# Kernel optimization log

Hardware: AMD Instinct MI355X
Metric: run time of the kernel (lower is better)

Reference implementation:

```python
import jax, jax.numpy as jnp
import numpy as np

H = 8
D_MODEL = 512
D_K = D_MODEL // H
NEG = -1e9


def setup_inputs() -> dict:
    key = jax.random.key(0)
    ks = jax.random.split(key, 11)
    B, S = 2, 2048
    scale = 1.0 / np.sqrt(D_MODEL)
    inp = {
        'query': jax.random.normal(ks[0], (B, S, D_MODEL), dtype=jnp.float32),
        'key': jax.random.normal(ks[1], (B, S, D_MODEL), dtype=jnp.float32),
        'value': jax.random.normal(ks[2], (B, S, D_MODEL), dtype=jnp.float32),
        'Wq': jax.random.normal(ks[3], (D_MODEL, D_MODEL), dtype=jnp.float32) * scale,
        'bq': jnp.zeros((D_MODEL,), dtype=jnp.float32),
        'Wk': jax.random.normal(ks[4], (D_MODEL, D_MODEL), dtype=jnp.float32) * scale,
        'bk': jnp.zeros((D_MODEL,), dtype=jnp.float32),
        'Wv': jax.random.normal(ks[5], (D_MODEL, D_MODEL), dtype=jnp.float32) * scale,
        'bv': jnp.zeros((D_MODEL,), dtype=jnp.float32),
        'Wo': jax.random.normal(ks[6], (D_MODEL, D_MODEL), dtype=jnp.float32) * scale,
        'bo': jnp.zeros((D_MODEL,), dtype=jnp.float32),
    }
    return inp


def reference(query, key, value, Wq, bq, Wk, bk, Wv, bv, Wo, bo):
    B, S, _ = query.shape
    # QKV projections (nn.Linear: x @ W.T + b), split into heads -> [B, H, S, D_K]
    def proj(x, W, b):
        return (x @ W.T + b).reshape(B, S, H, D_K).transpose(0, 2, 1, 3)

    q = proj(query, Wq, bq)
    k = proj(key, Wk, bk)
    v = proj(value, Wv, bv)

    scores = jnp.einsum('bhqd,bhkd->bhqk', q, k) / jnp.sqrt(jnp.float32(D_K))
    # diagonal mask (mask=True): token cannot attend to itself
    diag = jnp.eye(S, dtype=bool)
    scores = jnp.where(diag, NEG, scores)

    p_attn = jax.nn.softmax(scores, axis=-1)  # [B, H, S, S]
    x = jnp.einsum('bhqk,bhkd->bhqd', p_attn, v)
    x = x.transpose(0, 2, 1, 3).reshape(B, S, H * D_K)
    return x @ Wo.T + bo
```

## Files before the change

kernel.cpp:

```cpp
#include <hip/hip_runtime.h>
#include <hip/hip_bf16.h>
#include <math.h>

#define NUM_H 8
#define DK    64
#define DM    512
#define SEQ   2048
#define NB    2
#define MROWS (NB*SEQ)

typedef unsigned short u16;
typedef unsigned int   u32;
typedef __attribute__((ext_vector_type(8))) __bf16 bf16x8;
typedef __attribute__((ext_vector_type(4))) short  s16x4;
typedef __attribute__((ext_vector_type(4))) float  f32x4;

__device__ __forceinline__ u16 f2bf(float v) {
    union { __bf16 h; u16 u; } x; x.h = (__bf16)v; return x.u;
}
__device__ __forceinline__ u16 f2h(float v) {
    union { _Float16 h; u16 u; } x; x.h = (_Float16)v; return x.u;
}
__device__ __forceinline__ float h2f(u16 u) {
    union { u16 u; _Float16 h; } x; x.u = u; return (float)x.h;
}
__device__ __forceinline__ bf16x8 ld_bf8(const u16* p) {
    union { uint4 u; bf16x8 v; } t;
    t.u = *(const uint4*)p;
    return t.v;
}
__device__ __forceinline__ uint4 pack8bf(const float* f) {
    uint4 o;
    o.x = (u32)f2bf(f[0]) | ((u32)f2bf(f[1]) << 16);
    o.y = (u32)f2bf(f[2]) | ((u32)f2bf(f[3]) << 16);
    o.z = (u32)f2bf(f[4]) | ((u32)f2bf(f[5]) << 16);
    o.w = (u32)f2bf(f[6]) | ((u32)f2bf(f[7]) << 16);
    return o;
}
__device__ __forceinline__ float fexp2(float x) {
#if defined(__has_builtin) && __has_builtin(__builtin_amdgcn_exp2f)
    return __builtin_amdgcn_exp2f(x);
#else
    return exp2f(x);
#endif
}

__device__ __forceinline__ f32x4 mfma16bf(s16x4 a, s16x4 b, f32x4 c) {
#if defined(__has_builtin) && __has_builtin(__builtin_amdgcn_mfma_f32_16x16x16bf16_1k)
    return __builtin_amdgcn_mfma_f32_16x16x16bf16_1k(a, b, c, 0, 0, 0);
#else
    asm("v_mfma_f32_16x16x16_bf16 %0, %1, %2, %0" : "+v"(c) : "v"(a), "v"(b));
    return c;
#endif
}

__global__ __launch_bounds__(256) void convW(
    const float* __restrict__ Wq, const float* __restrict__ Wk,
    const float* __restrict__ Wv, const float* __restrict__ Wo,
    u16* __restrict__ Wscr)
{
    const int z = blockIdx.y;
    const float* src = (z == 0) ? Wq : (z == 1) ? Wk : (z == 2) ? Wv : Wo;
    u16* dst = Wscr + (size_t)z * 262144;
    int i = (blockIdx.x * 256 + threadIdx.x) * 8;
    float4 a = *(const float4*)(src + i);
    float4 b = *(const float4*)(src + i + 4);
    float f[8] = {a.x, a.y, a.z, a.w, b.x, b.y, b.z, b.w};
    *(uint4*)&dst[i] = pack8bf(f);
}

#define MODE_QK 0
#define MODE_VT 1
#define MODE_FIN 2

template<int MODE, bool INBF>
__device__ __forceinline__ void gemm_core(
    const void* __restrict__ Xv, const u16* __restrict__ Wb,
    const float* __restrict__ bias, void* __restrict__ outv,
    u16* As, u16* Bs, int row0, int col0)
{
    const int tid = threadIdx.x;
    const int lane = tid & 63, w = tid >> 6;
    const int ln15 = lane & 15, quad = lane >> 4;
    const int wm = (w >> 1) * 32, wn = (w & 1) * 32;

    f32x4 acc[2][2];
#pragma unroll
    for (int mt = 0; mt < 2; ++mt)
#pragma unroll
        for (int nt = 0; nt < 2; ++nt) acc[mt][nt] = (f32x4){0.f, 0.f, 0.f, 0.f};

    for (int kt = 0; kt < DM; kt += 64) {
        __syncthreads();
#pragma unroll
        for (int g = 0; g < 2; ++g) {
            int idx = g * 2048 + tid * 8;
            int r = idx >> 6, c = idx & 63;
            if (INBF) {
                *(uint4*)&As[r * 72 + c] =
                    *(const uint4*)((const u16*)Xv + (size_t)(row0 + r) * DM + kt + c);
            } else {
                const float* xp = (const float*)Xv + (size_t)(row0 + r) * DM + kt + c;
                float4 a = *(const float4*)xp;
                float4 b2 = *(const float4*)(xp + 4);
                float f[8] = {a.x, a.y, a.z, a.w, b2.x, b2.y, b2.z, b2.w};
                *(uint4*)&As[r * 72 + c] = pack8bf(f);
            }
        }
#pragma unroll
        for (int g = 0; g < 2; ++g) {
            int idx = g * 2048 + tid * 8;
            int r = idx >> 6, c = idx & 63;
            *(uint4*)&Bs[r * 72 + c] =
                *(const uint4*)(Wb + (size_t)(col0 + r) * DM + kt + c);
        }
        __syncthreads();

#pragma unroll
        for (int ks = 0; ks < 2; ++ks) {
            bf16x8 af[2], bfr[2];
#pragma unroll
            for (int mt = 0; mt < 2; ++mt)
                af[mt] = ld_bf8(&As[(wm + mt * 16 + ln15) * 72 + ks * 32 + quad * 8]);
#pragma unroll
            for (int nt = 0; nt < 2; ++nt)
                bfr[nt] = ld_bf8(&Bs[(wn + nt * 16 + ln15) * 72 + ks * 32 + quad * 8]);
#pragma unroll
            for (int mt = 0; mt < 2; ++mt)
#pragma unroll
                for (int nt = 0; nt < 2; ++nt)
                    acc[mt][nt] = __builtin_amdgcn_mfma_f32_16x16x32_bf16(
                        af[mt], bfr[nt], acc[mt][nt], 0, 0, 0);
        }
    }

    float bc[2];
#pragma unroll
    for (int nt = 0; nt < 2; ++nt) bc[nt] = bias[col0 + wn + nt * 16 + ln15];
    const int h = col0 >> 6;

    if (MODE == MODE_FIN) {
        float* outF = (float*)outv;
#pragma unroll
        for (int mt = 0; mt < 2; ++mt)
#pragma unroll
            for (int r = 0; r < 4; ++r) {
                int m = row0 + wm + mt * 16 + quad * 4 + r;
#pragma unroll
                for (int nt = 0; nt < 2; ++nt)
                    outF[(size_t)m * DM + col0 + wn + nt * 16 + ln15] = acc[mt][nt][r] + bc[nt];
            }
    } else if (MODE == MODE_QK) {
        u16* outB = (u16*)outv;
#pragma unroll
        for (int mt = 0; mt < 2; ++mt)
#pragma unroll
            for (int r = 0; r < 4; ++r) {
                int m = row0 + wm + mt * 16 + quad * 4 + r;
                int b = m >> 11, s2 = m & (SEQ - 1);
#pragma unroll
                for (int nt = 0; nt < 2; ++nt) {
                    int dk = wn + nt * 16 + ln15;
                    outB[((size_t)((b * NUM_H + h) * SEQ + s2)) * DK + dk] =
                        f2bf(acc[mt][nt][r] + bc[nt]);
                }
            }
    } else {
        u16* outB = (u16*)outv;
        __syncthreads();
#pragma unroll
        for (int mt = 0; mt < 2; ++mt)
#pragma unroll
            for (int nt = 0; nt < 2; ++nt) {
                int dk = wn + nt * 16 + ln15;
#pragma unroll
                for (int r = 0; r < 4; ++r) {
                    int sl = wm + mt * 16 + quad * 4 + r;
                    As[dk * 72 + sl] = f2bf(acc[mt][nt][r] + bc[nt]);
                }
            }
        __syncthreads();
        int dk = tid >> 2, ch = (tid & 3) * 16;
        int b = row0 >> 11, s0 = row0 & (SEQ - 1);
        size_t base = ((size_t)((b * NUM_H + h) * DK + dk)) * SEQ + s0 + ch;
        *(uint4*)&outB[base]     = *(const uint4*)&As[dk * 72 + ch];
        *(uint4*)&outB[base + 8] = *(const uint4*)&As[dk * 72 + ch + 8];
    }
}

__global__ __launch_bounds__(256) void qkv_mfma(
    const float* __restrict__ xq, const float* __restrict__ xk, const float* __restrict__ xv,
    const u16* __restrict__ Wscr,
    const float* __restrict__ b0, const float* __restrict__ b1, const float* __restrict__ b2,
    u16* __restrict__ oQ, u16* __restrict__ oK, u16* __restrict__ oVt)
{
    __shared__ u16 As[64 * 72];
    __shared__ u16 Bs[64 * 72];
    const int row0 = blockIdx.x * 64, col0 = blockIdx.y * 64;
    const int z = blockIdx.z;
    const u16* W = Wscr + (size_t)z * 262144;
    if (z == 2)
        gemm_core<MODE_VT, false>(xv, W, b2, oVt, As, Bs, row0, col0);
    else if (z == 0)
        gemm_core<MODE_QK, false>(xq, W, b0, oQ, As, Bs, row0, col0);
    else
        gemm_core<MODE_QK, false>(xk, W, b1, oK, As, Bs, row0, col0);
}

__global__ __launch_bounds__(256) void final_mfma(
    const u16* __restrict__ X, const u16* __restrict__ Wbf,
    const float* __restrict__ bias, float* __restrict__ out)
{
    __shared__ u16 As[64 * 72];
    __shared__ u16 Bs[64 * 72];
    gemm_core<MODE_FIN, true>(X, Wbf, bias, out, As, Bs,
                              blockIdx.x * 64, blockIdx.y * 64);
}

#define LSTR 72
#define SCL2  0.18033688f
#define BIA2 -5.7708020f
__global__ __launch_bounds__(256) void attn_mfma(
    const u16* __restrict__ Qg, const u16* __restrict__ Kg,
    const u16* __restrict__ Vtg, u16* __restrict__ Pd, float* __restrict__ Cl)
{
    __shared__ u16 Klds[64 * LSTR];
    __shared__ u16 Vtlds[64 * LSTR];

    const int tid = threadIdx.x;
    const int lane = tid & 63;
    const int w = tid >> 6;
    const int ln15 = lane & 15;
    const int quad = lane >> 4;
    const int bh = blockIdx.y;
    const int b = bh >> 3, h = bh & 7;
    const int qb = blockIdx.x * 64;
    const int z = blockIdx.z;
    const int k0 = z * (SEQ / 2), k1 = k0 + SEQ / 2;

    const u16* Qp = Qg + (size_t)bh * SEQ * DK;
    const u16* Kp = Kg + (size_t)bh * SEQ * DK;
    const u16* Vp = Vtg + (size_t)bh * DK * SEQ;

    const int myq = w * 16 + ln15;
    const int qrow = qb + myq;
    const bf16x8 qa0 = ld_bf8(&Qp[(size_t)qrow * DK + quad * 8]);
    const bf16x8 qa1 = ld_bf8(&Qp[(size_t)qrow * DK + 32 + quad * 8]);

    const bool mrow = (quad == (ln15 >> 2));
    const int  mr   = ln15 & 3;

    const s16x4 onesb = (s16x4){(short)0x3F80, (short)0x3F80,
                                (short)0x3F80, (short)0x3F80};

    f32x4 O[4];
    f32x4 Lacc = (f32x4){0.f, 0.f, 0.f, 0.f};
#pragma unroll
    for (int nt = 0; nt < 4; ++nt) O[nt] = (f32x4){0.f, 0.f, 0.f, 0.f};

    const int sr = tid >> 3;
    const int scl = (tid & 7) * 8;
    const u16* kp0 = &Kp[(size_t)sr * DK + scl];
    const u16* kp1 = &Kp[(size_t)(sr + 32) * DK + scl];
    const u16* vp0 = &Vp[(size_t)sr * SEQ + scl];
    const u16* vp1 = &Vp[(size_t)(sr + 32) * SEQ + scl];

    uint4 kreg0 = *(const uint4*)&kp0[(size_t)k0 * DK];
    uint4 kreg1 = *(const uint4*)&kp1[(size_t)k0 * DK];
    uint4 vreg0 = *(const uint4*)&vp0[k0];
    uint4 vreg1 = *(const uint4*)&vp1[k0];

    for (int kt = k0; kt < k1; kt += 64) {
        *(uint4*)&Klds[sr * LSTR + scl]         = kreg0;
        *(uint4*)&Klds[(sr + 32) * LSTR + scl]  = kreg1;
        *(uint4*)&Vtlds[sr * LSTR + scl]        = vreg0;
        *(uint4*)&Vtlds[(sr + 32) * LSTR + scl] = vreg1;
        __syncthreads();

        if (kt + 64 < k1) {
            kreg0 = *(const uint4*)&kp0[(size_t)(kt + 64) * DK];
            kreg1 = *(const uint4*)&kp1[(size_t)(kt + 64) * DK];
            vreg0 = *(const uint4*)&vp0[kt + 64];
            vreg1 = *(const uint4*)&vp1[kt + 64];
        }

        const bool diagt = (kt == qb);
        s16x4 pa[4];
#pragma unroll
        for (int nt2 = 0; nt2 < 4; ++nt2) {
            bf16x8 kb0 = ld_bf8(&Klds[(nt2 * 16 + ln15) * LSTR + quad * 8]);
            bf16x8 kb1 = ld_bf8(&Klds[(nt2 * 16 + ln15) * LSTR + 32 + quad * 8]);
            f32x4 zacc = (f32x4){0.f, 0.f, 0.f, 0.f};
            zacc = __builtin_amdgcn_mfma_f32_16x16x32_bf16(kb0, qa0, zacc, 0, 0, 0);
            zacc = __builtin_amdgcn_mfma_f32_16x16x32_bf16(kb1, qa1, zacc, 0, 0, 0);
            union { u16 u[4]; s16x4 v; } pk;
#pragma unroll
            for (int r = 0; r < 4; ++r)
                pk.u[r] = f2bf(fexp2(fmaf(zacc[r], SCL2, BIA2)));
            if (diagt && nt2 == w) {
#pragma unroll
                for (int r = 0; r < 4; ++r)
                    if (mrow && r == mr) pk.u[r] = 0;
            }
            pa[nt2] = pk.v;
        }

        const u16* vb_base = &Vtlds[ln15 * LSTR + quad * 4];
        __builtin_amdgcn_s_setprio(1);
#pragma unroll
        for (int nt2 = 0; nt2 < 4; ++nt2)
            Lacc = mfma16bf(pa[nt2], onesb, Lacc);
#pragma unroll
        for (int nt = 0; nt < 4; ++nt) {
#pragma unroll
            for (int nt2 = 0; nt2 < 4; ++nt2) {
                s16x4 vb = *(const s16x4*)&vb_base[nt * 16 * LSTR + nt2 * 16];
                O[nt] = mfma16bf(pa[nt2], vb, O[nt]);
            }
        }
        __builtin_amdgcn_s_setprio(0);
        __syncthreads();
    }

    if (ln15 == 0) {
#pragma unroll
        for (int r = 0; r < 4; ++r)
            Cl[(size_t)z * 32768 + bh * SEQ + qb + w * 16 + quad * 4 + r] = Lacc[r];
    }

#pragma unroll
    for (int r = 0; r < 4; ++r) {
        int s = qb + w * 16 + quad * 4 + r;
        size_t base = (size_t)z * 2097152 + ((size_t)(b * SEQ + s)) * DM + h * DK;
#pragma unroll
        for (int nt = 0; nt < 4; ++nt)
            Pd[base + nt * 16 + ln15] = f2h(O[nt][r] * 0.015625f);
    }
}

__global__ __launch_bounds__(256) void combine(
    const u16* __restrict__ Pd, const float* __restrict__ Cl, u16* __restrict__ C)
{
    int idx = (blockIdx.x * 256 + threadIdx.x) * 8;
    int row = idx >> 9, col = idx & 511;
    int b = row >> 11, s = row & (SEQ - 1), h = col >> 6;
    int bh = b * NUM_H + h;
    float lsum = Cl[bh * SEQ + s] + Cl[32768 + bh * SEQ + s];
    float sc = 64.f / lsum;
    uint4 u0 = *(const uint4*)&Pd[idx];
    uint4 u1 = *(const uint4*)&Pd[2097152 + idx];
    u32 a0[4] = {u0.x, u0.y, u0.z, u0.w};
    u32 a1[4] = {u1.x, u1.y, u1.z, u1.w};
    float f[8];
#pragma unroll
    for (int j = 0; j < 4; ++j) {
        f[2 * j]     = (h2f((u16)(a0[j] & 0xffff)) + h2f((u16)(a1[j] & 0xffff))) * sc;
        f[2 * j + 1] = (h2f((u16)(a0[j] >> 16))    + h2f((u16)(a1[j] >> 16)))    * sc;
    }
    *(uint4*)&C[idx] = pack8bf(f);
}

extern "C" void kernel_launch(void* const* d_in, const int* in_sizes, int n_in,
                              void* d_out, int out_size, void* d_ws, size_t ws_size,
                              hipStream_t stream) {
    const float* q  = (const float*)d_in[0];
    const float* k  = (const float*)d_in[1];
    const float* v  = (const float*)d_in[2];
    const float* Wq = (const float*)d_in[3];
    const float* bq = (const float*)d_in[4];
    const float* Wk = (const float*)d_in[5];
    const float* bk = (const float*)d_in[6];
    const float* Wv = (const float*)d_in[7];
    const float* bv = (const float*)d_in[8];
    const float* Wo = (const float*)d_in[9];
    const float* bo = (const float*)d_in[10];
    float* out = (float*)d_out;

    const size_t TSZ = (size_t)MROWS * DM;
    u16* Qb  = (u16*)d_ws;
    u16* Kb  = Qb + TSZ;
    u16* Vtb = Qb + 2 * TSZ;
    u16* CbU = Qb + 3 * TSZ;
    float* Cl  = (float*)CbU;
    u16*  Wscr = CbU + 131072;

    u16* Pd = (u16*)d_out;

    dim3 blk(256);
    hipLaunchKernelGGL(convW, dim3(128, 4), blk, 0, stream, Wq, Wk, Wv, Wo, Wscr);
    dim3 gq(MROWS / 64, DM / 64, 3);
    hipLaunchKernelGGL(qkv_mfma, gq, blk, 0, stream,
                       q, k, v, Wscr, bq, bk, bv, Qb, Kb, Vtb);
    dim3 ga(SEQ / 64, NB * NUM_H, 2);
    hipLaunchKernelGGL(attn_mfma, ga, blk, 0, stream, Qb, Kb, Vtb, Pd, Cl);
    hipLaunchKernelGGL(combine, dim3(1024), blk, 0, stream, Pd, Cl, Qb);
    dim3 gf(MROWS / 64, DM / 64);
    hipLaunchKernelGGL(final_mfma, gf, blk, 0, stream, Qb, Wscr + 3 * 262144, bo, out);
}
```

Measured before the change: 151.9 us.

## Split attention keys four ways and fuse split combine into output projection

Raises the key-dimension split of the attention kernel from 2 to 4, which doubles the number of attention blocks for better occupancy. It removes the separate combine kernel by having the output-projection GEMM load the four fp16 partial outputs, sum them with half2 adds, and scale each row by the reciprocal of the summed row denominators while staging the A tile. The cost is more partial-output traffic: four fp16 partial tensors are now written and read back. Summing in fp16 before scaling may also lose some precision. Partials move from the output buffer into workspace.

```diff
diff --git a/kernel.cpp b/kernel.cpp
--- a/kernel.cpp
+++ b/kernel.cpp
@@ -1,5 +1,6 @@
 #include <hip/hip_runtime.h>
 #include <hip/hip_bf16.h>
+#include <hip/hip_fp16.h>
 #include <math.h>
 
 #define NUM_H 8
@@ -8,6 +9,7 @@
 #define SEQ   2048
 #define NB    2
 #define MROWS (NB*SEQ)
+#define NZ    4
 
 typedef unsigned short u16;
 typedef unsigned int   u32;
@@ -20,9 +22,6 @@
 }
 __device__ __forceinline__ u16 f2h(float v) {
     union { _Float16 h; u16 u; } x; x.h = (_Float16)v; return x.u;
-}
-__device__ __forceinline__ float h2f(u16 u) {
-    union { u16 u; _Float16 h; } x; x.u = u; return (float)x.h;
 }
 __device__ __forceinline__ bf16x8 ld_bf8(const u16* p) {
     union { uint4 u; bf16x8 v; } t;
@@ -73,10 +72,11 @@
 #define MODE_VT 1
 #define MODE_FIN 2
 
-template<int MODE, bool INBF>
+template<int MODE>
 __device__ __forceinline__ void gemm_core(
     const void* __restrict__ Xv, const u16* __restrict__ Wb,
-    const float* __restrict__ bias, void* __restrict__ outv,
+    const float* __restrict__ bias, const float* __restrict__ ClP,
+    void* __restrict__ outv,
     u16* As, u16* Bs, int row0, int col0)
 {
     const int tid = threadIdx.x;
@@ -84,6 +84,13 @@
     const int ln15 = lane & 15, quad = lane >> 4;
     const int wm = (w >> 1) * 32, wn = (w & 1) * 32;
 
+    int cb0 = 0, cs0 = 0, cb1 = 0, cs1 = 0;
+    if (MODE == MODE_FIN) {
+        int m0 = row0 + (tid >> 3), m1 = m0 + 32;
+        cb0 = (m0 >> 11) * NUM_H; cs0 = m0 & (SEQ - 1);
+        cb1 = (m1 >> 11) * NUM_H; cs1 = m1 & (SEQ - 1);
+    }
+
     f32x4 acc[2][2];
 #pragma unroll
     for (int mt = 0; mt < 2; ++mt)
@@ -92,14 +99,40 @@
 
     for (int kt = 0; kt < DM; kt += 64) {
         __syncthreads();
-#pragma unroll
-        for (int g = 0; g < 2; ++g) {
-            int idx = g * 2048 + tid * 8;
-            int r = idx >> 6, c = idx & 63;
-            if (INBF) {
-                *(uint4*)&As[r * 72 + c] =
-                    *(const uint4*)((const u16*)Xv + (size_t)(row0 + r) * DM + kt + c);
-            } else {
+        if (MODE == MODE_FIN) {
+            const int h = kt >> 6;
+            float l0 = ClP[(cb0 + h) * SEQ + cs0] + ClP[32768 + (cb0 + h) * SEQ + cs0]
+                     + ClP[65536 + (cb0 + h) * SEQ + cs0] + ClP[98304 + (cb0 + h) * SEQ + cs0];
+            float l1 = ClP[(cb1 + h) * SEQ + cs1] + ClP[32768 + (cb1 + h) * SEQ + cs1]
+                     + ClP[65536 + (cb1 + h) * SEQ + cs1] + ClP[98304 + (cb1 + h) * SEQ + cs1];
+            float scr[2] = {64.f / l0, 64.f / l1};
+#pragma unroll
+            for (int g = 0; g < 2; ++g) {
+                int r = g * 32 + (tid >> 3);
+                int c = (tid & 7) * 8;
+                const u16* pp = (const u16*)Xv + (size_t)(row0 + r) * DM + kt + c;
+                union { uint4 u; __half2 h2[4]; } u0, u1, u2, u3;
+                u0.u = *(const uint4*)pp;
+                u1.u = *(const uint4*)(pp + 2097152);
+                u2.u = *(const uint4*)(pp + 2 * 2097152);
+                u3.u = *(const uint4*)(pp + 3 * 2097152);
+                float f[8];
+                float sc = scr[g];
+#pragma unroll
+                for (int j = 0; j < 4; ++j) {
+                    __half2 s2 = __hadd2(__hadd2(u0.h2[j], u1.h2[j]),
+                                         __hadd2(u2.h2[j], u3.h2[j]));
+                    float2 fl = __half22float2(s2);
+                    f[2 * j]     = fl.x * sc;
+                    f[2 * j + 1] = fl.y * sc;
+                }
+                *(uint4*)&As[r * 72 + c] = pack8bf(f);
+            }
+        } else {
+#pragma unroll
+            for (int g = 0; g < 2; ++g) {
+                int idx = g * 2048 + tid * 8;
+                int r = idx >> 6, c = idx & 63;
                 const float* xp = (const float*)Xv + (size_t)(row0 + r) * DM + kt + c;
                 float4 a = *(const float4*)xp;
                 float4 b2 = *(const float4*)(xp + 4);
@@ -200,21 +233,22 @@
     const int z = blockIdx.z;
     const u16* W = Wscr + (size_t)z * 262144;
     if (z == 2)
-        gemm_core<MODE_VT, false>(xv, W, b2, oVt, As, Bs, row0, col0);
+        gemm_core<MODE_VT>(xv, W, b2, nullptr, oVt, As, Bs, row0, col0);
     else if (z == 0)
-        gemm_core<MODE_QK, false>(xq, W, b0, oQ, As, Bs, row0, col0);
+        gemm_core<MODE_QK>(xq, W, b0, nullptr, oQ, As, Bs, row0, col0);
     else
-        gemm_core<MODE_QK, false>(xk, W, b1, oK, As, Bs, row0, col0);
+        gemm_core<MODE_QK>(xk, W, b1, nullptr, oK, As, Bs, row0, col0);
 }
 
 __global__ __launch_bounds__(256) void final_mfma(
-    const u16* __restrict__ X, const u16* __restrict__ Wbf,
-    const float* __restrict__ bias, float* __restrict__ out)
+    const u16* __restrict__ Pd, const u16* __restrict__ Wbf,
+    const float* __restrict__ Cl, const float* __restrict__ bias,
+    float* __restrict__ out)
 {
     __shared__ u16 As[64 * 72];
     __shared__ u16 Bs[64 * 72];
-    gemm_core<MODE_FIN, true>(X, Wbf, bias, out, As, Bs,
-                              blockIdx.x * 64, blockIdx.y * 64);
+    gemm_core<MODE_FIN>(Pd, Wbf, bias, Cl, out, As, Bs,
+                        blockIdx.x * 64, blockIdx.y * 64);
 }
 
 #define LSTR 72
@@ -236,7 +270,7 @@
     const int b = bh >> 3, h = bh & 7;
     const int qb = blockIdx.x * 64;
     const int z = blockIdx.z;
-    const int k0 = z * (SEQ / 2), k1 = k0 + SEQ / 2;
+    const int k0 = z * (SEQ / NZ), k1 = k0 + SEQ / NZ;
 
     const u16* Qp = Qg + (size_t)bh * SEQ * DK;
     const u16* Kp = Kg + (size_t)bh * SEQ * DK;
@@ -336,28 +370,6 @@
         for (int nt = 0; nt < 4; ++nt)
             Pd[base + nt * 16 + ln15] = f2h(O[nt][r] * 0.015625f);
     }
-}
-
-__global__ __launch_bounds__(256) void combine(
-    const u16* __restrict__ Pd, const float* __restrict__ Cl, u16* __restrict__ C)
-{
-    int idx = (blockIdx.x * 256 + threadIdx.x) * 8;
-    int row = idx >> 9, col = idx & 511;
-    int b = row >> 11, s = row & (SEQ - 1), h = col >> 6;
-    int bh = b * NUM_H + h;
-    float lsum = Cl[bh * SEQ + s] + Cl[32768 + bh * SEQ + s];
-    float sc = 64.f / lsum;
-    uint4 u0 = *(const uint4*)&Pd[idx];
-    uint4 u1 = *(const uint4*)&Pd[2097152 + idx];
-    u32 a0[4] = {u0.x, u0.y, u0.z, u0.w};
-    u32 a1[4] = {u1.x, u1.y, u1.z, u1.w};
-    float f[8];
-#pragma unroll
-    for (int j = 0; j < 4; ++j) {
-        f[2 * j]     = (h2f((u16)(a0[j] & 0xffff)) + h2f((u16)(a1[j] & 0xffff))) * sc;
-        f[2 * j + 1] = (h2f((u16)(a0[j] >> 16))    + h2f((u16)(a1[j] >> 16)))    * sc;
-    }
-    *(uint4*)&C[idx] = pack8bf(f);
 }
 
 extern "C" void kernel_launch(void* const* d_in, const int* in_sizes, int n_in,
@@ -377,23 +389,20 @@
     float* out = (float*)d_out;
 
     const size_t TSZ = (size_t)MROWS * DM;
-    u16* Qb  = (u16*)d_ws;
-    u16* Kb  = Qb + TSZ;
-    u16* Vtb = Qb + 2 * TSZ;
-    u16* CbU = Qb + 3 * TSZ;
-    float* Cl  = (float*)CbU;
-    u16*  Wscr = CbU + 131072;
-
-    u16* Pd = (u16*)d_out;
+    u16* Qb   = (u16*)d_ws;
+    u16* Kb   = Qb + TSZ;
+    u16* Vtb  = Qb + 2 * TSZ;
+    float* Cl = (float*)(Qb + 3 * TSZ);
+    u16* Wscr = (u16*)(Cl + 131072);
+    u16* Pd   = Wscr + 4 * 262144;
 
     dim3 blk(256);
     hipLaunchKernelGGL(convW, dim3(128, 4), blk, 0, stream, Wq, Wk, Wv, Wo, Wscr);
     dim3 gq(MROWS / 64, DM / 64, 3);
     hipLaunchKernelGGL(qkv_mfma, gq, blk, 0, stream,
                        q, k, v, Wscr, bq, bk, bv, Qb, Kb, Vtb);
-    dim3 ga(SEQ / 64, NB * NUM_H, 2);
+    dim3 ga(SEQ / 64, NB * NUM_H, NZ);
     hipLaunchKernelGGL(attn_mfma, ga, blk, 0, stream, Qb, Kb, Vtb, Pd, Cl);
-    hipLaunchKernelGGL(combine, dim3(1024), blk, 0, stream, Pd, Cl, Qb);
     dim3 gf(MROWS / 64, DM / 64);
-    hipLaunchKernelGGL(final_mfma, gf, blk, 0, stream, Qb, Wscr + 3 * 262144, bo, out);
-}
+    hipLaunchKernelGGL(final_mfma, gf, blk, 0, stream, Pd, Wscr + 3 * 262144, Cl, bo, out);
+}
```

Measured after the change: 149.9 us. Within noise of the previous version (-1.3%).
